# Kernel tuning notes

Hardware: AMD Instinct MI355X
Metric: run time of the kernel (lower is better)

## Reference

```python
import jax, jax.numpy as jnp
import numpy as np

B = 2048       # number of samples
A = 64         # max agents per sample (static)
E = 128        # h_dim
H = 8          # num_heads
DH = E // H    # head dim = 16


def _agents():
    # deterministic ragged pattern covering 1..64; sum = 66560
    return jnp.asarray(((np.arange(B) * 7) % A) + 1, dtype=jnp.int32)


def setup_inputs() -> dict:
    key = jax.random.key(0)
    ks = jax.random.split(key, 6)
    agents = _agents()
    total = int(np.sum(((np.arange(B) * 7) % A) + 1))  # 66560
    att_in = jax.random.normal(ks[0], (total, E), dtype=jnp.float32)
    # nn.MultiheadAttention parameters
    in_proj_w = jax.random.normal(ks[1], (3 * E, E), dtype=jnp.float32) * 0.02
    in_proj_b = jnp.zeros((3 * E,), dtype=jnp.float32)
    out_proj_w = jax.random.normal(ks[2], (E, E), dtype=jnp.float32) * 0.02
    out_proj_b = jnp.zeros((E,), dtype=jnp.float32)
    return {
        "att_in": att_in,
        "in_proj_w": in_proj_w,
        "in_proj_b": in_proj_b,
        "out_proj_w": out_proj_w,
        "out_proj_b": out_proj_b,
        "agents_per_sample": agents,
    }


def reference(att_in, in_proj_w, in_proj_b, out_proj_w, out_proj_b, agents_per_sample):
    total = att_in.shape[0]
    # ---- pad ragged [total, E] -> [B, A, E] ----
    sample_ids = jnp.repeat(jnp.arange(B), agents_per_sample, total_repeat_length=total)
    offsets = jnp.concatenate([jnp.zeros((1,), jnp.int32), jnp.cumsum(agents_per_sample)[:-1]])
    slot_ids = jnp.arange(total) - offsets[sample_ids]
    padded = jnp.zeros((B, A, E), att_in.dtype).at[sample_ids, slot_ids].set(att_in)
    key_valid = jnp.arange(A)[None, :] < agents_per_sample[:, None]  # [B, A]

    # ---- multi-head self-attention (dropout disabled / eval mode) ----
    qkv = padded @ in_proj_w.T + in_proj_b            # [B, A, 3E]
    q, k, v = jnp.split(qkv, 3, axis=-1)
    def heads(x):
        return x.reshape(B, A, H, DH).transpose(0, 2, 1, 3)  # [B, H, A, DH]
    q, k, v = heads(q), heads(k), heads(v)
    scores = jnp.einsum("bhqd,bhkd->bhqk", q, k) / jnp.sqrt(jnp.float32(DH))
    scores = jnp.where(key_valid[:, None, None, :], scores, jnp.float32(-1e9))
    attn = jax.nn.softmax(scores, axis=-1)            # [B, H, A, A]
    ctx = jnp.einsum("bhqk,bhkd->bhqd", attn, v)      # [B, H, A, DH]
    ctx = ctx.transpose(0, 2, 1, 3).reshape(B, A, E)
    out = ctx @ out_proj_w.T + out_proj_b             # [B, A, E]

    # ---- unpad back to flat ragged [total, E] ----
    return out[sample_ids, slot_ids]
```

## Files before the change

kernel.cpp:

```cpp
#include <hip/hip_runtime.h>

#define NB    2048
#define AMAX  64
#define EDIM  128
#define TOTAL 66560
#define DHEAD 16
#define KVSTR 20
#define XSTR  129
#define LSTR  136
#define WELEM 65536
#define NSLOT 8192

typedef _Float16 f16x8 __attribute__((ext_vector_type(8)));
typedef _Float16 f16x4 __attribute__((ext_vector_type(4)));
typedef float    f32x4 __attribute__((ext_vector_type(4)));

__global__ __launch_bounds__(256) void prep_kernel(const int* __restrict__ ag,
                                                   int* __restrict__ offs,
                                                   const float* __restrict__ win,
                                                   const float* __restrict__ wout,
                                                   _Float16* __restrict__ wh,
                                                   int4* __restrict__ dsc,
                                                   int* __restrict__ nblk) {
    if (blockIdx.x == 0) {
        __shared__ int part[256];
        __shared__ int cnt[8];
        __shared__ int rk[8];
        __shared__ int cb[8];
        const int t = threadIdx.x;
        int myn[8], loc[8];
        int s = 0;
#pragma unroll
        for (int i = 0; i < 8; ++i) { myn[i] = ag[t * 8 + i]; loc[i] = s; s += myn[i]; }
        part[t] = s;
        __syncthreads();
        for (int d = 1; d < 256; d <<= 1) {
            int v = (t >= d) ? part[t - d] : 0;
            __syncthreads();
            part[t] += v;
            __syncthreads();
        }
        const int base = (t == 0) ? 0 : part[t - 1];
#pragma unroll
        for (int i = 0; i < 8; ++i) offs[t * 8 + i] = base + loc[i];

        if (dsc != nullptr) {
            for (int j = t; j < NSLOT; j += 256)
                dsc[j] = make_int4(0, 0, -(j + 1), j & 3);
            if (t < 8) { cnt[t] = 0; rk[t] = 0; }
            __syncthreads();
#pragma unroll
            for (int i = 0; i < 8; ++i)
                atomicAdd(&cnt[(myn[i] + 15) >> 4], 1);
            __syncthreads();
            if (t == 0) {
                const int c4 = cnt[4], c3 = cnt[3], c2 = cnt[2], c1 = cnt[1];
                const int p31 = (c3 < c1) ? c3 : c1;
                const int q2 = c2 >> 1, odd2 = c2 & 1;
                int u1a = c1 - p31; const int cap = odd2 ? 2 : 0;
                if (u1a > cap) u1a = cap; if (u1a < 0) u1a = 0;
                const int rem1 = c1 - p31 - u1a;
                cb[4] = 0; cb[3] = c4; cb[2] = c4 + c3;
                cb[0] = p31; cb[1] = u1a;
                nblk[0] = c4 + c3 + q2 + odd2 + ((rem1 + 3) >> 2);
            }
            __syncthreads();
#pragma unroll
            for (int i = 0; i < 8; ++i) {
                const int sid = t * 8 + i, n = myn[i], off = base + loc[i];
                const int nt = (n + 15) >> 4;
                const int r = atomicAdd(&rk[nt], 1);
                int blk, s0;
                if (nt == 4)      { blk = r;            s0 = 0; }
                else if (nt == 3) { blk = cb[3] + r;    s0 = 0; }
                else if (nt == 2) { blk = cb[2] + (r >> 1); s0 = (r & 1) << 1; }
                else {
                    const int p31 = cb[0], u1a = cb[1], c2 = cnt[2];
                    if (r < p31)            { blk = cb[3] + r;          s0 = 3; }
                    else if (r < p31 + u1a) { blk = cb[2] + (c2 >> 1);  s0 = 2 + (r - p31); }
                    else {
                        const int rr = r - p31 - u1a;
                        blk = cb[2] + (c2 >> 1) + (c2 & 1) + (rr >> 2);
                        s0 = rr & 3;
                    }
                }
                for (int tt = 0; tt < nt; ++tt) {
                    int nrem = n - tt * 16; if (nrem > 16) nrem = 16;
                    dsc[blk * 4 + s0 + tt] = make_int4(off + tt * 16, nrem, sid, s0 | (n << 8));
                }
            }
        }
    } else {
        const int base = (blockIdx.x - 1) * 1024 + threadIdx.x * 4;
        const float4 v = (base < 49152) ? *(const float4*)(win + base)
                                        : *(const float4*)(wout + (base - 49152));
        f16x4 h;
        h[0] = (_Float16)v.x; h[1] = (_Float16)v.y;
        h[2] = (_Float16)v.z; h[3] = (_Float16)v.w;
        *(f16x4*)(wh + base) = h;
    }
}

__global__ __launch_bounds__(256, 2) void fused_attn_kernel(
    const float*    __restrict__ x,
    const _Float16* __restrict__ winh,
    const float*    __restrict__ bin,
    const _Float16* __restrict__ woh,
    const float*    __restrict__ bout,
    const int4*     __restrict__ dsc,
    const int*      __restrict__ nblk,
    float*          __restrict__ out)
{
    __shared__ __align__(16) _Float16 xs[AMAX * LSTR];

    const int b = blockIdx.x;
    if (b >= nblk[0]) return;
    const int tid  = threadIdx.x;
    const int lane = tid & 63;
    const int wid  = __builtin_amdgcn_readfirstlane(tid >> 6);
    const int l15  = lane & 15;
    const int quad = lane >> 4;

    int4 dd[4];
#pragma unroll
    for (int t = 0; t < 4; ++t) dd[t] = dsc[b * 4 + t];

    f16x8 wq[2][4], wk[2][4], wv[2][4];
    float bqa[2][4], bka[2][4], bva[2];
#pragma unroll
    for (int m = 0; m < 2; ++m) {
        const int h = wid * 2 + m;
#pragma unroll
        for (int ks = 0; ks < 4; ++ks) {
            wq[m][ks] = *(const f16x8*)(winh + (size_t)(h * 16 + l15) * EDIM + ks * 32 + quad * 8);
            wk[m][ks] = *(const f16x8*)(winh + (size_t)(128 + h * 16 + l15) * EDIM + ks * 32 + quad * 8);
            wv[m][ks] = *(const f16x8*)(winh + (size_t)(256 + h * 16 + l15) * EDIM + ks * 32 + quad * 8);
        }
        const float4 bq = *(const float4*)(bin + h * 16 + quad * 4);
        const float4 bk = *(const float4*)(bin + 128 + h * 16 + quad * 4);
        bqa[m][0]=bq.x; bqa[m][1]=bq.y; bqa[m][2]=bq.z; bqa[m][3]=bq.w;
        bka[m][0]=bk.x; bka[m][1]=bk.y; bka[m][2]=bk.z; bka[m][3]=bk.w;
        bva[m] = bin[256 + h * 16 + l15];
    }

    {
        const int rr = tid >> 4, c8 = tid & 15;
#pragma unroll
        for (int t = 0; t < 4; ++t) {
            f16x8 hv = {};
            if (rr < dd[t].y) {
                const float* xr = x + (size_t)(dd[t].x + rr) * EDIM + c8 * 8;
                const float4 a0 = *(const float4*)xr;
                const float4 a1 = *(const float4*)(xr + 4);
                hv[0]=(_Float16)a0.x; hv[1]=(_Float16)a0.y; hv[2]=(_Float16)a0.z; hv[3]=(_Float16)a0.w;
                hv[4]=(_Float16)a1.x; hv[5]=(_Float16)a1.y; hv[6]=(_Float16)a1.z; hv[7]=(_Float16)a1.w;
            }
            *(f16x8*)(xs + (t * 16 + rr) * LSTR + c8 * 8) = hv;
        }
    }
    __syncthreads();

    const float QSC = 0.25f * 1.44269504088896f;
    f16x4 qf[2][4], kf[2][4], vf[2][4];
#pragma unroll
    for (int kt = 0; kt < 4; ++kt) {
        f16x8 xf[4];
#pragma unroll
        for (int ks = 0; ks < 4; ++ks)
            xf[ks] = *(const f16x8*)(xs + (kt * 16 + l15) * LSTR + ks * 32 + quad * 8);
#pragma unroll
        for (int m = 0; m < 2; ++m) {
            f32x4 aq = (f32x4){0.f,0.f,0.f,0.f};
            f32x4 ak = (f32x4){0.f,0.f,0.f,0.f};
            f32x4 av = (f32x4){0.f,0.f,0.f,0.f};
#pragma unroll
            for (int ks = 0; ks < 4; ++ks) {
                aq = __builtin_amdgcn_mfma_f32_16x16x32_f16(wq[m][ks], xf[ks], aq, 0, 0, 0);
                ak = __builtin_amdgcn_mfma_f32_16x16x32_f16(wk[m][ks], xf[ks], ak, 0, 0, 0);
                av = __builtin_amdgcn_mfma_f32_16x16x32_f16(xf[ks], wv[m][ks], av, 0, 0, 0);
            }
#pragma unroll
            for (int r = 0; r < 4; ++r) {
                qf[m][kt][r] = (_Float16)((aq[r] + bqa[m][r]) * QSC);
                kf[m][kt][r] = (_Float16)(ak[r] + bka[m][r]);
                vf[m][kt][r] = (_Float16)(av[r] + bva[m]);
            }
        }
    }

    f16x4 ctxf[2][4] = {};
#pragma unroll
    for (int qt = 0; qt < 4; ++qt) {
        const int baseq = dd[qt].w & 255;
        const int nsq   = dd[qt].w >> 8;
        const int sidq  = dd[qt].z;
        bool act[4];
#pragma unroll
        for (int kt = 0; kt < 4; ++kt) act[kt] = (dd[kt].z == sidq);

        f32x4 sv0[4], sv1[4];
#pragma unroll
        for (int kt = 0; kt < 4; ++kt) if (act[kt]) {
            sv0[kt] = __builtin_amdgcn_mfma_f32_16x16x16f16(
                          kf[0][kt], qf[0][qt], (f32x4){0.f,0.f,0.f,0.f}, 0, 0, 0);
            sv1[kt] = __builtin_amdgcn_mfma_f32_16x16x16f16(
                          kf[1][kt], qf[1][qt], (f32x4){0.f,0.f,0.f,0.f}, 0, 0, 0);
        }
        float t0[4], t1[4];
#pragma unroll
        for (int kt = 0; kt < 4; ++kt) { t0[kt] = 0.f; t1[kt] = 0.f; }
#pragma unroll
        for (int kt = 0; kt < 4; ++kt) if (act[kt]) {
            float s0 = 0.f, s1 = 0.f;
#pragma unroll
            for (int r = 0; r < 4; ++r) {
                const int key = (kt - baseq) * 16 + quad * 4 + r;
                const float p0 = (key < nsq) ? __builtin_amdgcn_exp2f(sv0[kt][r]) : 0.f;
                const float p1 = (key < nsq) ? __builtin_amdgcn_exp2f(sv1[kt][r]) : 0.f;
                s0 += p0; sv0[kt][r] = p0;
                s1 += p1; sv1[kt][r] = p1;
            }
            t0[kt] = s0; t1[kt] = s1;
        }
        float ls0 = (t0[0] + t0[1]) + (t0[2] + t0[3]);
        float ls1 = (t1[0] + t1[1]) + (t1[2] + t1[3]);
        ls0 += __shfl_xor(ls0, 16, 64);
        ls1 += __shfl_xor(ls1, 16, 64);
        ls0 += __shfl_xor(ls0, 32, 64);
        ls1 += __shfl_xor(ls1, 32, 64);
        const float inv0 = __builtin_amdgcn_rcpf(ls0);
        const float inv1 = __builtin_amdgcn_rcpf(ls1);
        f16x4 pf0[4], pf1[4];
#pragma unroll
        for (int kt = 0; kt < 4; ++kt) if (act[kt]) {
#pragma unroll
            for (int r = 0; r < 4; ++r) {
                pf0[kt][r] = (_Float16)(sv0[kt][r] * inv0);
                pf1[kt][r] = (_Float16)(sv1[kt][r] * inv1);
            }
        }
        f32x4 a0A = (f32x4){0.f,0.f,0.f,0.f}, a0B = (f32x4){0.f,0.f,0.f,0.f};
        f32x4 a1A = (f32x4){0.f,0.f,0.f,0.f}, a1B = (f32x4){0.f,0.f,0.f,0.f};
#pragma unroll
        for (int kt = 0; kt < 4; ++kt) if (act[kt]) {
            if ((kt & 1) == 0) {
                a0A = __builtin_amdgcn_mfma_f32_16x16x16f16(pf0[kt], vf[0][kt], a0A, 0, 0, 0);
                a1A = __builtin_amdgcn_mfma_f32_16x16x16f16(pf1[kt], vf[1][kt], a1A, 0, 0, 0);
            } else {
                a0B = __builtin_amdgcn_mfma_f32_16x16x16f16(pf0[kt], vf[0][kt], a0B, 0, 0, 0);
                a1B = __builtin_amdgcn_mfma_f32_16x16x16f16(pf1[kt], vf[1][kt], a1B, 0, 0, 0);
            }
        }
#pragma unroll
        for (int r = 0; r < 4; ++r) {
            ctxf[0][qt][r] = (_Float16)(a0A[r] + a0B[r]);
            ctxf[1][qt][r] = (_Float16)(a1A[r] + a1B[r]);
        }
    }

    __syncthreads();
#pragma unroll
    for (int m = 0; m < 2; ++m) {
        const int h = wid * 2 + m;
#pragma unroll
        for (int qt = 0; qt < 4; ++qt) {
#pragma unroll
            for (int r = 0; r < 4; ++r)
                xs[(qt * 16 + quad * 4 + r) * LSTR + h * 16 + l15] = ctxf[m][qt][r];
        }
    }
    __syncthreads();

    {
        f32x4 oacc[4][2];
#pragma unroll
        for (int t = 0; t < 4; ++t) { oacc[t][0] = (f32x4){0.f,0.f,0.f,0.f}; oacc[t][1] = (f32x4){0.f,0.f,0.f,0.f}; }
#pragma unroll
        for (int ks = 0; ks < 4; ++ks) {
            f16x8 cf[2];
#pragma unroll
            for (int c2 = 0; c2 < 2; ++c2)
                cf[c2] = *(const f16x8*)(woh + (wid * 32 + c2 * 16 + l15) * EDIM + ks * 32 + quad * 8);
#pragma unroll
            for (int t = 0; t < 4; ++t) {
                const f16x8 rf = *(const f16x8*)(xs + (t * 16 + l15) * LSTR + ks * 32 + quad * 8);
                oacc[t][0] = __builtin_amdgcn_mfma_f32_16x16x32_f16(cf[0], rf, oacc[t][0], 0, 0, 0);
                oacc[t][1] = __builtin_amdgcn_mfma_f32_16x16x32_f16(cf[1], rf, oacc[t][1], 0, 0, 0);
            }
        }
        const float4 bo0 = *(const float4*)(bout + wid * 32 + quad * 4);
        const float4 bo1 = *(const float4*)(bout + wid * 32 + 16 + quad * 4);
#pragma unroll
        for (int t = 0; t < 4; ++t) {
            if (l15 < dd[t].y) {
                float* orow = out + (size_t)(dd[t].x + l15) * EDIM + wid * 32;
                *(float4*)(orow + quad * 4) =
                    make_float4(oacc[t][0][0] + bo0.x, oacc[t][0][1] + bo0.y,
                                oacc[t][0][2] + bo0.z, oacc[t][0][3] + bo0.w);
                *(float4*)(orow + 16 + quad * 4) =
                    make_float4(oacc[t][1][0] + bo1.x, oacc[t][1][1] + bo1.y,
                                oacc[t][1][2] + bo1.z, oacc[t][1][3] + bo1.w);
            }
        }
    }
}

__global__ __launch_bounds__(256, 2) void attn_fused_kernel(
    const float* __restrict__ x, const float* __restrict__ win,
    const float* __restrict__ bin, const float* __restrict__ wout,
    const float* __restrict__ bout, const int* __restrict__ ag,
    const int* __restrict__ offs, float* __restrict__ out)
{
    __shared__ __align__(16) float xs[AMAX * XSTR];
    __shared__ __align__(16) float kvs[8][AMAX * KVSTR];
    const int b = blockIdx.x, n = ag[b], off = offs[b];
    const int tid = threadIdx.x, lane = tid & 63;
    const int wid = __builtin_amdgcn_readfirstlane(tid >> 6);
#pragma unroll
    for (int it = 0; it < 8; ++it) {
        const int f4 = it * 256 + tid;
        const int r = f4 >> 5, c = (f4 & 31) << 2;
        float4 v = make_float4(0.f, 0.f, 0.f, 0.f);
        if (r < n) v = *(const float4*)(x + (size_t)(off + r) * EDIM + c);
        float* d = xs + r * XSTR + c;
        d[0]=v.x; d[1]=v.y; d[2]=v.z; d[3]=v.w;
    }
    __syncthreads();
    float* kw = kvs[wid*2+0]; float* vw = kvs[wid*2+1];
    const float* xrow = xs + lane * XSTR;
    float ctxk[2][DHEAD];
#pragma unroll
    for (int m = 0; m < 2; ++m) {
        const int h = wid * 2 + m;
        float qa[DHEAD], ka[DHEAD], va[DHEAD];
#pragma unroll
        for (int d = 0; d < DHEAD; ++d) { qa[d]=0.f; ka[d]=0.f; va[d]=0.f; }
        const float* wq = win + (size_t)(h*DHEAD)*EDIM;
        const float* wk = win + (size_t)(EDIM + h*DHEAD)*EDIM;
        const float* wv = win + (size_t)(2*EDIM + h*DHEAD)*EDIM;
        for (int k = 0; k < EDIM; ++k) {
            const float xv = xrow[k];
#pragma unroll
            for (int d = 0; d < DHEAD; ++d) {
                qa[d] = fmaf(xv, wq[d*EDIM+k], qa[d]);
                ka[d] = fmaf(xv, wk[d*EDIM+k], ka[d]);
                va[d] = fmaf(xv, wv[d*EDIM+k], va[d]);
            }
        }
#pragma unroll
        for (int d = 0; d < DHEAD; ++d) {
            qa[d] = (qa[d] + bin[h*DHEAD+d]) * 0.25f;
            ka[d] += bin[EDIM + h*DHEAD + d];
            va[d] += bin[2*EDIM + h*DHEAD + d];
        }
#pragma unroll
        for (int d = 0; d < DHEAD; ++d) { kw[lane*KVSTR+d] = ka[d]; vw[lane*KVSTR+d] = va[d]; }
        float mrun = -1e30f, lrun = 0.f, cacc[DHEAD];
#pragma unroll
        for (int d = 0; d < DHEAD; ++d) cacc[d] = 0.f;
        const int nch = (n + 15) >> 4;
        for (int ch = 0; ch < nch; ++ch) {
            const int jb = ch << 4;
            float s[16], p[16];
#pragma unroll
            for (int jj = 0; jj < 16; ++jj) {
                const float4* kr = (const float4*)(kw + (jb + jj) * KVSTR);
                const float4 k0=kr[0],k1=kr[1],k2=kr[2],k3=kr[3];
                const float kk[16] = {k0.x,k0.y,k0.z,k0.w,k1.x,k1.y,k1.z,k1.w,
                                      k2.x,k2.y,k2.z,k2.w,k3.x,k3.y,k3.z,k3.w};
                float a = 0.f;
#pragma unroll
                for (int d = 0; d < DHEAD; ++d) a = fmaf(qa[d], kk[d], a);
                s[jj] = (jb + jj < n) ? a : -1e30f;
            }
            float mc = s[0];
#pragma unroll
            for (int jj = 1; jj < 16; ++jj) mc = fmaxf(mc, s[jj]);
            const float mnew = fmaxf(mrun, mc);
            const float alpha = __expf(mrun - mnew);
            float psum = 0.f;
#pragma unroll
            for (int jj = 0; jj < 16; ++jj) { p[jj] = __expf(s[jj]-mnew); psum += p[jj]; }
            lrun = fmaf(lrun, alpha, psum);
#pragma unroll
            for (int d = 0; d < DHEAD; ++d) cacc[d] *= alpha;
#pragma unroll
            for (int jj = 0; jj < 16; ++jj) {
                const float4* vr = (const float4*)(vw + (jb + jj) * KVSTR);
                const float4 v0=vr[0],v1=vr[1],v2=vr[2],v3=vr[3];
                const float vv[16] = {v0.x,v0.y,v0.z,v0.w,v1.x,v1.y,v1.z,v1.w,
                                      v2.x,v2.y,v2.z,v2.w,v3.x,v3.y,v3.z,v3.w};
                const float pj = p[jj];
#pragma unroll
                for (int d = 0; d < DHEAD; ++d) cacc[d] = fmaf(pj, vv[d], cacc[d]);
            }
            mrun = mnew;
        }
        const float inv = 1.0f / lrun;
#pragma unroll
        for (int d = 0; d < DHEAD; ++d) ctxk[m][d] = cacc[d] * inv;
    }
    __syncthreads();
#pragma unroll
    for (int m = 0; m < 2; ++m) {
        const int h = wid * 2 + m;
#pragma unroll
        for (int d = 0; d < DHEAD; ++d) xs[lane*XSTR + h*DHEAD + d] = ctxk[m][d];
    }
    __syncthreads();
    const int c0 = wid * 32;
#pragma unroll
    for (int ct = 0; ct < 4; ++ct) {
        const int cc = c0 + ct * 8;
        float a8[8];
#pragma unroll
        for (int j = 0; j < 8; ++j) a8[j] = 0.f;
#pragma unroll 4
        for (int e = 0; e < EDIM; ++e) {
            const float cv = xrow[e];
#pragma unroll
            for (int j = 0; j < 8; ++j) a8[j] = fmaf(cv, wout[(size_t)(cc+j)*EDIM+e], a8[j]);
        }
        if (lane < n) {
            float* orow = out + (size_t)(off + lane) * EDIM + cc;
#pragma unroll
            for (int j = 0; j < 8; ++j) orow[j] = a8[j] + bout[cc+j];
        }
    }
}

extern "C" void kernel_launch(void* const* d_in, const int* in_sizes, int n_in,
                              void* d_out, int out_size, void* d_ws, size_t ws_size,
                              hipStream_t stream) {
    const float* x   = (const float*)d_in[0];
    const float* win = (const float*)d_in[1];
    const float* bin = (const float*)d_in[2];
    const float* wo  = (const float*)d_in[3];
    const float* bo  = (const float*)d_in[4];
    const int*   ag  = (const int*)d_in[5];
    float* out = (float*)d_out;

    const size_t need = (size_t)WELEM * sizeof(_Float16) + (size_t)NSLOT * sizeof(int4)
                      + NB * sizeof(int) + 4 * sizeof(int);
    if (ws_size >= need) {
        _Float16* wh = (_Float16*)d_ws;
        int4* dsc = (int4*)(wh + WELEM);
        int* offs = (int*)(dsc + NSLOT);
        int* nblk = offs + NB;
        prep_kernel<<<65, 256, 0, stream>>>(ag, offs, win, wo, wh, dsc, nblk);
        fused_attn_kernel<<<NB, 256, 0, stream>>>(x, wh, bin, wh + 49152, bo, dsc, nblk, out);
    } else {
        int* offs = (int*)d_ws;
        prep_kernel<<<1, 256, 0, stream>>>(ag, offs, nullptr, nullptr, nullptr, nullptr, nullptr);
        attn_fused_kernel<<<NB, 256, 0, stream>>>(x, win, bin, wo, bo, ag, offs, out);
    }
}
```

Before: 128.5 us.

## Make fused attention kernel persistent with double-buffered prefetch of next unit

The attention kernel becomes persistent, launching a fixed grid of 512 blocks that loop over work units with a stride of the grid size. Weights and biases are loaded into registers once per block instead of once per unit. The next unit's input rows are fetched from global memory into registers before the current unit's compute and written to a second LDS buffer afterwards, so load latency overlaps with compute. The cost is doubled LDS use, extra live registers for the prefetch, and fewer blocks in flight, which may hurt occupancy or load balance.

```diff
diff --git a/kernel.cpp b/kernel.cpp
--- a/kernel.cpp
+++ b/kernel.cpp
@@ -10,6 +10,8 @@
 #define LSTR  136
 #define WELEM 65536
 #define NSLOT 8192
+#define GRID  512
+#define UHALF (64 * LSTR)
 
 typedef _Float16 f16x8 __attribute__((ext_vector_type(8)));
 typedef _Float16 f16x4 __attribute__((ext_vector_type(4)));
@@ -111,19 +113,17 @@
     const int*      __restrict__ nblk,
     float*          __restrict__ out)
 {
-    __shared__ __align__(16) _Float16 xs[AMAX * LSTR];
-
-    const int b = blockIdx.x;
-    if (b >= nblk[0]) return;
+    __shared__ __align__(16) _Float16 xsb[2 * UHALF];
+
+    const int NU   = nblk[0];
+    int u          = blockIdx.x;
+    if (u >= NU) return;
     const int tid  = threadIdx.x;
     const int lane = tid & 63;
     const int wid  = __builtin_amdgcn_readfirstlane(tid >> 6);
     const int l15  = lane & 15;
     const int quad = lane >> 4;
-
-    int4 dd[4];
-#pragma unroll
-    for (int t = 0; t < 4; ++t) dd[t] = dsc[b * 4 + t];
+    const int rr   = tid >> 4, c8 = tid & 15;
 
     f16x8 wq[2][4], wk[2][4], wv[2][4];
     float bqa[2][4], bka[2][4], bva[2];
@@ -142,166 +142,208 @@
         bka[m][0]=bk.x; bka[m][1]=bk.y; bka[m][2]=bk.z; bka[m][3]=bk.w;
         bva[m] = bin[256 + h * 16 + l15];
     }
-
-    {
-        const int rr = tid >> 4, c8 = tid & 15;
-#pragma unroll
-        for (int t = 0; t < 4; ++t) {
-            f16x8 hv = {};
-            if (rr < dd[t].y) {
-                const float* xr = x + (size_t)(dd[t].x + rr) * EDIM + c8 * 8;
-                const float4 a0 = *(const float4*)xr;
-                const float4 a1 = *(const float4*)(xr + 4);
-                hv[0]=(_Float16)a0.x; hv[1]=(_Float16)a0.y; hv[2]=(_Float16)a0.z; hv[3]=(_Float16)a0.w;
-                hv[4]=(_Float16)a1.x; hv[5]=(_Float16)a1.y; hv[6]=(_Float16)a1.z; hv[7]=(_Float16)a1.w;
-            }
-            *(f16x8*)(xs + (t * 16 + rr) * LSTR + c8 * 8) = hv;
-        }
+    const float4 bo0 = *(const float4*)(bout + wid * 32 + quad * 4);
+    const float4 bo1 = *(const float4*)(bout + wid * 32 + 16 + quad * 4);
+
+    int4 dd[4];
+#pragma unroll
+    for (int t = 0; t < 4; ++t) dd[t] = dsc[u * 4 + t];
+    _Float16* cur = xsb;
+    _Float16* nxt = xsb + UHALF;
+#pragma unroll
+    for (int t = 0; t < 4; ++t) {
+        f16x8 hv = {};
+        if (rr < dd[t].y) {
+            const float* xr = x + (size_t)(dd[t].x + rr) * EDIM + c8 * 8;
+            const float4 a0 = *(const float4*)xr;
+            const float4 a1 = *(const float4*)(xr + 4);
+            hv[0]=(_Float16)a0.x; hv[1]=(_Float16)a0.y; hv[2]=(_Float16)a0.z; hv[3]=(_Float16)a0.w;
+            hv[4]=(_Float16)a1.x; hv[5]=(_Float16)a1.y; hv[6]=(_Float16)a1.z; hv[7]=(_Float16)a1.w;
+        }
+        *(f16x8*)(cur + (t * 16 + rr) * LSTR + c8 * 8) = hv;
     }
     __syncthreads();
 
     const float QSC = 0.25f * 1.44269504088896f;
-    f16x4 qf[2][4], kf[2][4], vf[2][4];
-#pragma unroll
-    for (int kt = 0; kt < 4; ++kt) {
-        f16x8 xf[4];
-#pragma unroll
-        for (int ks = 0; ks < 4; ++ks)
-            xf[ks] = *(const f16x8*)(xs + (kt * 16 + l15) * LSTR + ks * 32 + quad * 8);
+
+    while (true) {
+        const int un = u + GRID;
+        const bool nval = un < NU;
+        int4 nd[4];
+        float4 na[4], nb[4];
+        if (nval) {
+#pragma unroll
+            for (int t = 0; t < 4; ++t) nd[t] = dsc[un * 4 + t];
+#pragma unroll
+            for (int t = 0; t < 4; ++t) {
+                na[t] = make_float4(0.f, 0.f, 0.f, 0.f);
+                nb[t] = make_float4(0.f, 0.f, 0.f, 0.f);
+                if (rr < nd[t].y) {
+                    const float* xr = x + (size_t)(nd[t].x + rr) * EDIM + c8 * 8;
+                    na[t] = *(const float4*)xr;
+                    nb[t] = *(const float4*)(xr + 4);
+                }
+            }
+        }
+
+        f16x4 qf[2][4], kf[2][4], vf[2][4];
+#pragma unroll
+        for (int kt = 0; kt < 4; ++kt) {
+            f16x8 xf[4];
+#pragma unroll
+            for (int ks = 0; ks < 4; ++ks)
+                xf[ks] = *(const f16x8*)(cur + (kt * 16 + l15) * LSTR + ks * 32 + quad * 8);
+#pragma unroll
+            for (int m = 0; m < 2; ++m) {
+                f32x4 aq = (f32x4){0.f,0.f,0.f,0.f};
+                f32x4 ak = (f32x4){0.f,0.f,0.f,0.f};
+                f32x4 av = (f32x4){0.f,0.f,0.f,0.f};
+#pragma unroll
+                for (int ks = 0; ks < 4; ++ks) {
+                    aq = __builtin_amdgcn_mfma_f32_16x16x32_f16(wq[m][ks], xf[ks], aq, 0, 0, 0);
+                    ak = __builtin_amdgcn_mfma_f32_16x16x32_f16(wk[m][ks], xf[ks], ak, 0, 0, 0);
+                    av = __builtin_amdgcn_mfma_f32_16x16x32_f16(xf[ks], wv[m][ks], av, 0, 0, 0);
+                }
+#pragma unroll
+                for (int r = 0; r < 4; ++r) {
+                    qf[m][kt][r] = (_Float16)((aq[r] + bqa[m][r]) * QSC);
+                    kf[m][kt][r] = (_Float16)(ak[r] + bka[m][r]);
+                    vf[m][kt][r] = (_Float16)(av[r] + bva[m]);
+                }
+            }
+        }
+
+        f16x4 ctxf[2][4] = {};
+#pragma unroll
+        for (int qt = 0; qt < 4; ++qt) {
+            const int baseq = dd[qt].w & 255;
+            const int nsq   = dd[qt].w >> 8;
+            const int sidq  = dd[qt].z;
+            bool act[4];
+#pragma unroll
+            for (int kt = 0; kt < 4; ++kt) act[kt] = (dd[kt].z == sidq);
+
+            f32x4 sv0[4], sv1[4];
+#pragma unroll
+            for (int kt = 0; kt < 4; ++kt) if (act[kt]) {
+                sv0[kt] = __builtin_amdgcn_mfma_f32_16x16x16f16(
+                              kf[0][kt], qf[0][qt], (f32x4){0.f,0.f,0.f,0.f}, 0, 0, 0);
+                sv1[kt] = __builtin_amdgcn_mfma_f32_16x16x16f16(
+                              kf[1][kt], qf[1][qt], (f32x4){0.f,0.f,0.f,0.f}, 0, 0, 0);
+            }
+            float t0[4], t1[4];
+#pragma unroll
+            for (int kt = 0; kt < 4; ++kt) { t0[kt] = 0.f; t1[kt] = 0.f; }
+#pragma unroll
+            for (int kt = 0; kt < 4; ++kt) if (act[kt]) {
+                float s0 = 0.f, s1 = 0.f;
+#pragma unroll
+                for (int r = 0; r < 4; ++r) {
+                    const int key = (kt - baseq) * 16 + quad * 4 + r;
+                    const float p0 = (key < nsq) ? __builtin_amdgcn_exp2f(sv0[kt][r]) : 0.f;
+                    const float p1 = (key < nsq) ? __builtin_amdgcn_exp2f(sv1[kt][r]) : 0.f;
+                    s0 += p0; sv0[kt][r] = p0;
+                    s1 += p1; sv1[kt][r] = p1;
+                }
+                t0[kt] = s0; t1[kt] = s1;
+            }
+            float ls0 = (t0[0] + t0[1]) + (t0[2] + t0[3]);
+            float ls1 = (t1[0] + t1[1]) + (t1[2] + t1[3]);
+            ls0 += __shfl_xor(ls0, 16, 64);
+            ls1 += __shfl_xor(ls1, 16, 64);
+            ls0 += __shfl_xor(ls0, 32, 64);
+            ls1 += __shfl_xor(ls1, 32, 64);
+            const float inv0 = __builtin_amdgcn_rcpf(ls0);
+            const float inv1 = __builtin_amdgcn_rcpf(ls1);
+            f16x4 pf0[4], pf1[4];
+#pragma unroll
+            for (int kt = 0; kt < 4; ++kt) if (act[kt]) {
+#pragma unroll
+                for (int r = 0; r < 4; ++r) {
+                    pf0[kt][r] = (_Float16)(sv0[kt][r] * inv0);
+                    pf1[kt][r] = (_Float16)(sv1[kt][r] * inv1);
+                }
+            }
+            f32x4 a0A = (f32x4){0.f,0.f,0.f,0.f}, a0B = (f32x4){0.f,0.f,0.f,0.f};
+            f32x4 a1A = (f32x4){0.f,0.f,0.f,0.f}, a1B = (f32x4){0.f,0.f,0.f,0.f};
+#pragma unroll
+            for (int kt = 0; kt < 4; ++kt) if (act[kt]) {
+                if ((kt & 1) == 0) {
+                    a0A = __builtin_amdgcn_mfma_f32_16x16x16f16(pf0[kt], vf[0][kt], a0A, 0, 0, 0);
+                    a1A = __builtin_amdgcn_mfma_f32_16x16x16f16(pf1[kt], vf[1][kt], a1A, 0, 0, 0);
+                } else {
+                    a0B = __builtin_amdgcn_mfma_f32_16x16x16f16(pf0[kt], vf[0][kt], a0B, 0, 0, 0);
+                    a1B = __builtin_amdgcn_mfma_f32_16x16x16f16(pf1[kt], vf[1][kt], a1B, 0, 0, 0);
+                }
+            }
+#pragma unroll
+            for (int r = 0; r < 4; ++r) {
+                ctxf[0][qt][r] = (_Float16)(a0A[r] + a0B[r]);
+                ctxf[1][qt][r] = (_Float16)(a1A[r] + a1B[r]);
+            }
+        }
+
+        __syncthreads();
+
 #pragma unroll
         for (int m = 0; m < 2; ++m) {
-            f32x4 aq = (f32x4){0.f,0.f,0.f,0.f};
-            f32x4 ak = (f32x4){0.f,0.f,0.f,0.f};
-            f32x4 av = (f32x4){0.f,0.f,0.f,0.f};
+            const int h = wid * 2 + m;
+#pragma unroll
+            for (int qt = 0; qt < 4; ++qt) {
+#pragma unroll
+                for (int r = 0; r < 4; ++r)
+                    cur[(qt * 16 + quad * 4 + r) * LSTR + h * 16 + l15] = ctxf[m][qt][r];
+            }
+        }
+        if (nval) {
+#pragma unroll
+            for (int t = 0; t < 4; ++t) {
+                f16x8 hv;
+                hv[0]=(_Float16)na[t].x; hv[1]=(_Float16)na[t].y;
+                hv[2]=(_Float16)na[t].z; hv[3]=(_Float16)na[t].w;
+                hv[4]=(_Float16)nb[t].x; hv[5]=(_Float16)nb[t].y;
+                hv[6]=(_Float16)nb[t].z; hv[7]=(_Float16)nb[t].w;
+                *(f16x8*)(nxt + (t * 16 + rr) * LSTR + c8 * 8) = hv;
+            }
+        }
+        __syncthreads();
+
+        {
+            f32x4 oacc[4][2];
+#pragma unroll
+            for (int t = 0; t < 4; ++t) { oacc[t][0] = (f32x4){0.f,0.f,0.f,0.f}; oacc[t][1] = (f32x4){0.f,0.f,0.f,0.f}; }
 #pragma unroll
             for (int ks = 0; ks < 4; ++ks) {
-                aq = __builtin_amdgcn_mfma_f32_16x16x32_f16(wq[m][ks], xf[ks], aq, 0, 0, 0);
-                ak = __builtin_amdgcn_mfma_f32_16x16x32_f16(wk[m][ks], xf[ks], ak, 0, 0, 0);
-                av = __builtin_amdgcn_mfma_f32_16x16x32_f16(xf[ks], wv[m][ks], av, 0, 0, 0);
-            }
-#pragma unroll
-            for (int r = 0; r < 4; ++r) {
-                qf[m][kt][r] = (_Float16)((aq[r] + bqa[m][r]) * QSC);
-                kf[m][kt][r] = (_Float16)(ak[r] + bka[m][r]);
-                vf[m][kt][r] = (_Float16)(av[r] + bva[m]);
-            }
-        }
-    }
-
-    f16x4 ctxf[2][4] = {};
-#pragma unroll
-    for (int qt = 0; qt < 4; ++qt) {
-        const int baseq = dd[qt].w & 255;
-        const int nsq   = dd[qt].w >> 8;
-        const int sidq  = dd[qt].z;
-        bool act[4];
-#pragma unroll
-        for (int kt = 0; kt < 4; ++kt) act[kt] = (dd[kt].z == sidq);
-
-        f32x4 sv0[4], sv1[4];
-#pragma unroll
-        for (int kt = 0; kt < 4; ++kt) if (act[kt]) {
-            sv0[kt] = __builtin_amdgcn_mfma_f32_16x16x16f16(
-                          kf[0][kt], qf[0][qt], (f32x4){0.f,0.f,0.f,0.f}, 0, 0, 0);
-            sv1[kt] = __builtin_amdgcn_mfma_f32_16x16x16f16(
-                          kf[1][kt], qf[1][qt], (f32x4){0.f,0.f,0.f,0.f}, 0, 0, 0);
-        }
-        float t0[4], t1[4];
-#pragma unroll
-        for (int kt = 0; kt < 4; ++kt) { t0[kt] = 0.f; t1[kt] = 0.f; }
-#pragma unroll
-        for (int kt = 0; kt < 4; ++kt) if (act[kt]) {
-            float s0 = 0.f, s1 = 0.f;
-#pragma unroll
-            for (int r = 0; r < 4; ++r) {
-                const int key = (kt - baseq) * 16 + quad * 4 + r;
-                const float p0 = (key < nsq) ? __builtin_amdgcn_exp2f(sv0[kt][r]) : 0.f;
-                const float p1 = (key < nsq) ? __builtin_amdgcn_exp2f(sv1[kt][r]) : 0.f;
-                s0 += p0; sv0[kt][r] = p0;
-                s1 += p1; sv1[kt][r] = p1;
-            }
-            t0[kt] = s0; t1[kt] = s1;
-        }
-        float ls0 = (t0[0] + t0[1]) + (t0[2] + t0[3]);
-        float ls1 = (t1[0] + t1[1]) + (t1[2] + t1[3]);
-        ls0 += __shfl_xor(ls0, 16, 64);
-        ls1 += __shfl_xor(ls1, 16, 64);
-        ls0 += __shfl_xor(ls0, 32, 64);
-        ls1 += __shfl_xor(ls1, 32, 64);
-        const float inv0 = __builtin_amdgcn_rcpf(ls0);
-        const float inv1 = __builtin_amdgcn_rcpf(ls1);
-        f16x4 pf0[4], pf1[4];
-#pragma unroll
-        for (int kt = 0; kt < 4; ++kt) if (act[kt]) {
-#pragma unroll
-            for (int r = 0; r < 4; ++r) {
-                pf0[kt][r] = (_Float16)(sv0[kt][r] * inv0);
-                pf1[kt][r] = (_Float16)(sv1[kt][r] * inv1);
-            }
-        }
-        f32x4 a0A = (f32x4){0.f,0.f,0.f,0.f}, a0B = (f32x4){0.f,0.f,0.f,0.f};
-        f32x4 a1A = (f32x4){0.f,0.f,0.f,0.f}, a1B = (f32x4){0.f,0.f,0.f,0.f};
-#pragma unroll
-        for (int kt = 0; kt < 4; ++kt) if (act[kt]) {
-            if ((kt & 1) == 0) {
-                a0A = __builtin_amdgcn_mfma_f32_16x16x16f16(pf0[kt], vf[0][kt], a0A, 0, 0, 0);
-                a1A = __builtin_amdgcn_mfma_f32_16x16x16f16(pf1[kt], vf[1][kt], a1A, 0, 0, 0);
-            } else {
-                a0B = __builtin_amdgcn_mfma_f32_16x16x16f16(pf0[kt], vf[0][kt], a0B, 0, 0, 0);
-                a1B = __builtin_amdgcn_mfma_f32_16x16x16f16(pf1[kt], vf[1][kt], a1B, 0, 0, 0);
-            }
-        }
-#pragma unroll
-        for (int r = 0; r < 4; ++r) {
-            ctxf[0][qt][r] = (_Float16)(a0A[r] + a0B[r]);
-            ctxf[1][qt][r] = (_Float16)(a1A[r] + a1B[r]);
-        }
-    }
-
-    __syncthreads();
-#pragma unroll
-    for (int m = 0; m < 2; ++m) {
-        const int h = wid * 2 + m;
-#pragma unroll
-        for (int qt = 0; qt < 4; ++qt) {
-#pragma unroll
-            for (int r = 0; r < 4; ++r)
-                xs[(qt * 16 + quad * 4 + r) * LSTR + h * 16 + l15] = ctxf[m][qt][r];
-        }
-    }
-    __syncthreads();
-
-    {
-        f32x4 oacc[4][2];
-#pragma unroll
-        for (int t = 0; t < 4; ++t) { oacc[t][0] = (f32x4){0.f,0.f,0.f,0.f}; oacc[t][1] = (f32x4){0.f,0.f,0.f,0.f}; }
-#pragma unroll
-        for (int ks = 0; ks < 4; ++ks) {
-            f16x8 cf[2];
-#pragma unroll
-            for (int c2 = 0; c2 < 2; ++c2)
-                cf[c2] = *(const f16x8*)(woh + (wid * 32 + c2 * 16 + l15) * EDIM + ks * 32 + quad * 8);
+                f16x8 cf[2];
+#pragma unroll
+                for (int c2 = 0; c2 < 2; ++c2)
+                    cf[c2] = *(const f16x8*)(woh + (wid * 32 + c2 * 16 + l15) * EDIM + ks * 32 + quad * 8);
+#pragma unroll
+                for (int t = 0; t < 4; ++t) {
+                    const f16x8 rf = *(const f16x8*)(cur + (t * 16 + l15) * LSTR + ks * 32 + quad * 8);
+                    oacc[t][0] = __builtin_amdgcn_mfma_f32_16x16x32_f16(cf[0], rf, oacc[t][0], 0, 0, 0);
+                    oacc[t][1] = __builtin_amdgcn_mfma_f32_16x16x32_f16(cf[1], rf, oacc[t][1], 0, 0, 0);
+                }
+            }
 #pragma unroll
             for (int t = 0; t < 4; ++t) {
-                const f16x8 rf = *(const f16x8*)(xs + (t * 16 + l15) * LSTR + ks * 32 + quad * 8);
-                oacc[t][0] = __builtin_amdgcn_mfma_f32_16x16x32_f16(cf[0], rf, oacc[t][0], 0, 0, 0);
-                oacc[t][1] = __builtin_amdgcn_mfma_f32_16x16x32_f16(cf[1], rf, oacc[t][1], 0, 0, 0);
-            }
-        }
-        const float4 bo0 = *(const float4*)(bout + wid * 32 + quad * 4);
-        const float4 bo1 = *(const float4*)(bout + wid * 32 + 16 + quad * 4);
-#pragma unroll
-        for (int t = 0; t < 4; ++t) {
-            if (l15 < dd[t].y) {
-                float* orow = out + (size_t)(dd[t].x + l15) * EDIM + wid * 32;
-                *(float4*)(orow + quad * 4) =
-                    make_float4(oacc[t][0][0] + bo0.x, oacc[t][0][1] + bo0.y,
-                                oacc[t][0][2] + bo0.z, oacc[t][0][3] + bo0.w);
-                *(float4*)(orow + 16 + quad * 4) =
-                    make_float4(oacc[t][1][0] + bo1.x, oacc[t][1][1] + bo1.y,
-                                oacc[t][1][2] + bo1.z, oacc[t][1][3] + bo1.w);
-            }
-        }
+                if (l15 < dd[t].y) {
+                    float* orow = out + (size_t)(dd[t].x + l15) * EDIM + wid * 32;
+                    *(float4*)(orow + quad * 4) =
+                        make_float4(oacc[t][0][0] + bo0.x, oacc[t][0][1] + bo0.y,
+                                    oacc[t][0][2] + bo0.z, oacc[t][0][3] + bo0.w);
+                    *(float4*)(orow + 16 + quad * 4) =
+                        make_float4(oacc[t][1][0] + bo1.x, oacc[t][1][1] + bo1.y,
+                                    oacc[t][1][2] + bo1.z, oacc[t][1][3] + bo1.w);
+                }
+            }
+        }
+
+        if (!nval) break;
+        u = un;
+#pragma unroll
+        for (int t = 0; t < 4; ++t) dd[t] = nd[t];
+        _Float16* tmp = cur; cur = nxt; nxt = tmp;
     }
 }
 
@@ -448,7 +490,7 @@
         int* offs = (int*)(dsc + NSLOT);
         int* nblk = offs + NB;
         prep_kernel<<<65, 256, 0, stream>>>(ag, offs, win, wo, wh, dsc, nblk);
-        fused_attn_kernel<<<NB, 256, 0, stream>>>(x, wh, bin, wh + 49152, bo, dsc, nblk, out);
+        fused_attn_kernel<<<GRID, 256, 0, stream>>>(x, wh, bin, wh + 49152, bo, dsc, nblk, out);
     } else {
         int* offs = (int*)d_ws;
         prep_kernel<<<1, 256, 0, stream>>>(ag, offs, nullptr, nullptr, nullptr, nullptr, nullptr);
```

Result: slower. 188.5 us (+46.7%).
